# Kernel optimization log

Hardware: AMD Instinct MI355X
Metric: run time of the kernel (lower is better)

## Reference

```python
import jax, jax.numpy as jnp
import numpy as np

N_NODES = 100000
N_EDGES = 3200000
IN_F = 128
EDGE_F = 16
OUT_F = 128
EDGE_IMPORTANCE = 1.0


def setup_inputs() -> dict:
    key = jax.random.key(0)
    k1, k2, k3, k4, k5 = jax.random.split(key, 5)
    x = jax.random.normal(k1, (N_NODES, IN_F), dtype=jnp.float32)
    edge_index = jax.random.randint(k2, (2, N_EDGES), 0, N_NODES, dtype=jnp.int64)
    edge_attr = jax.random.normal(k3, (N_EDGES, EDGE_F), dtype=jnp.float32)
    # nn.Linear(in_features + edge_features, out_features): weight [OUT_F, IN_F+EDGE_F]
    fan_in = IN_F + EDGE_F
    bound = 1.0 / np.sqrt(fan_in)
    W = jax.random.uniform(k4, (OUT_F, fan_in), dtype=jnp.float32, minval=-bound, maxval=bound)
    b = jax.random.uniform(k5, (OUT_F,), dtype=jnp.float32, minval=-bound, maxval=bound)
    return {"x": x, "edge_index": edge_index, "edge_attr": edge_attr, "W": W, "b": b}


def reference(x, edge_index, edge_attr, W, b):
    row, col = edge_index[0], edge_index[1]
    # Linear on concat([x[row], edge_attr*imp]) == x[row] @ Wx.T + edge @ We.T + b
    Wx = W[:, :IN_F]           # [OUT_F, IN_F]
    We = W[:, IN_F:]           # [OUT_F, EDGE_F]
    atom_feats = x[row]                                     # [E, IN_F] gather
    edge_feats = edge_attr * EDGE_IMPORTANCE                # [E, EDGE_F]
    updated = (jnp.einsum('ei,oi->eo', atom_feats, Wx)
               + jnp.einsum('ej,oj->eo', edge_feats, We)
               + b)                                         # [E, OUT_F]
    # scatter_mean by destination node col, dim_size = N
    sums = jax.ops.segment_sum(updated, col, num_segments=N_NODES)        # [N, OUT_F]
    counts = jax.ops.segment_sum(jnp.ones((updated.shape[0],), updated.dtype),
                                 col, num_segments=N_NODES)               # [N]
    denom = jnp.maximum(counts, 1.0)[:, None]
    return sums / denom
```

## Files before the change

kernel.cpp:

```cpp
#include <hip/hip_runtime.h>

#define N_NODES 100000
#define N_EDGES 3200000
#define IN_F    128
#define EDGE_F  16
#define OUT_F   128
#define K_TOT   144

typedef float f32x4 __attribute__((ext_vector_type(4)));
typedef int   i32x2 __attribute__((ext_vector_type(2)));


__global__ void count_k(const int* __restrict__ col, int* __restrict__ counts,
                        int* __restrict__ rank) {
    int e = blockIdx.x * blockDim.x + threadIdx.x;
    if (e < N_EDGES) {
        int c = __builtin_nontemporal_load(col + e);
        int r = atomicAdd(&counts[c], 1);
        __builtin_nontemporal_store(r, rank + e);
    }
}

__global__ void scan1_k(const int* __restrict__ counts, int* __restrict__ offsets,
                        int* __restrict__ partials) {
    __shared__ int s[512];
    int i = blockIdx.x * 512 + threadIdx.x;
    int v = (i < N_NODES) ? counts[i] : 0;
    s[threadIdx.x] = v;
    __syncthreads();
    for (int d = 1; d < 512; d <<= 1) {
        int t = (threadIdx.x >= d) ? s[threadIdx.x - d] : 0;
        __syncthreads();
        s[threadIdx.x] += t;
        __syncthreads();
    }
    if (i < N_NODES) offsets[i] = s[threadIdx.x] - v;
    if (threadIdx.x == 511) partials[blockIdx.x] = s[511];
}

__global__ void scan2_k(int* partials) {
    __shared__ int s[256];
    int v = (threadIdx.x < 196) ? partials[threadIdx.x] : 0;
    s[threadIdx.x] = v;
    __syncthreads();
    for (int d = 1; d < 256; d <<= 1) {
        int t = (threadIdx.x >= d) ? s[threadIdx.x - d] : 0;
        __syncthreads();
        s[threadIdx.x] += t;
        __syncthreads();
    }
    if (threadIdx.x < 196) partials[threadIdx.x] = s[threadIdx.x] - v;
}

__global__ void scan3_k(int* __restrict__ offsets, const int* __restrict__ partials) {
    int i = blockIdx.x * 512 + threadIdx.x;
    if (i < N_NODES) offsets[i] += partials[blockIdx.x];
    if (i == 0) offsets[N_NODES] = N_EDGES;
}

__global__ void fill_k(const int* __restrict__ col, const int* __restrict__ row,
                       const int* __restrict__ rank, const int* __restrict__ offsets,
                       int2* __restrict__ csr2) {
    int e = blockIdx.x * blockDim.x + threadIdx.x;
    if (e < N_EDGES) {
        int c  = __builtin_nontemporal_load(col + e);
        int rk = __builtin_nontemporal_load(rank + e);
        int rw = __builtin_nontemporal_load(row + e);
        int pos = offsets[c] + rk;
        i32x2 v; v.x = e; v.y = rw;
        __builtin_nontemporal_store(v, ((i32x2*)csr2) + pos);
    }
}

__global__ __launch_bounds__(256) void gather_k(
        const float* __restrict__ x, const float* __restrict__ ea,
        const int* __restrict__ offsets, const int* __restrict__ csr2,
        float* __restrict__ Sx, float* __restrict__ Se) {
    const int wave = threadIdx.x >> 6;
    const int lane = threadIdx.x & 63;
    const int n = blockIdx.x * 4 + wave;

    const int off0 = offsets[n];
    const int deg  = offsets[n + 1] - off0;

    const int half = lane >> 5;
    const int l31  = lane & 31;
    const int eg16 = lane >> 2;
    const int l3   = lane & 3;

    f32x4 ax = {0.f, 0.f, 0.f, 0.f};
    f32x4 se = {0.f, 0.f, 0.f, 0.f};

    for (int base = 0; base < deg; base += 64) {
        int m = deg - base; if (m > 64) m = 64;
        int e = 0, r = 0;
        if (lane < m) {
            i32x2 er = __builtin_nontemporal_load(
                ((const i32x2*)csr2) + off0 + base + lane);
            e = er.x; r = er.y;
        }
        int j = 0;
        for (; j + 16 <= m; j += 16) {
            int r0 = __shfl(r, j + 0  + half);
            int r1 = __shfl(r, j + 2  + half);
            int r2 = __shfl(r, j + 4  + half);
            int r3 = __shfl(r, j + 6  + half);
            int r4 = __shfl(r, j + 8  + half);
            int r5 = __shfl(r, j + 10 + half);
            int r6 = __shfl(r, j + 12 + half);
            int r7 = __shfl(r, j + 14 + half);
            int ej = __shfl(e, j + eg16);
            f32x4 v0 = ((const f32x4*)(x + (size_t)r0 * IN_F))[l31];
            f32x4 v1 = ((const f32x4*)(x + (size_t)r1 * IN_F))[l31];
            f32x4 v2 = ((const f32x4*)(x + (size_t)r2 * IN_F))[l31];
            f32x4 v3 = ((const f32x4*)(x + (size_t)r3 * IN_F))[l31];
            f32x4 v4 = ((const f32x4*)(x + (size_t)r4 * IN_F))[l31];
            f32x4 v5 = ((const f32x4*)(x + (size_t)r5 * IN_F))[l31];
            f32x4 v6 = ((const f32x4*)(x + (size_t)r6 * IN_F))[l31];
            f32x4 v7 = ((const f32x4*)(x + (size_t)r7 * IN_F))[l31];
            f32x4 w  = __builtin_nontemporal_load(
                ((const f32x4*)ea) + (size_t)ej * 4 + l3);
            ax += (v0 + v1) + (v2 + v3) + (v4 + v5) + (v6 + v7);
            se += w;
        }
        for (; j < m; j += 2) {
            int rj = __shfl(r, j + half);
            if (j + half < m) {
                f32x4 v = ((const f32x4*)(x + (size_t)rj * IN_F))[l31];
                ax += v;
            }
            int eg = eg16 & 1;
            int ej = __shfl(e, j + eg);
            if (lane < 8 && (j + eg) < m) {
                f32x4 w = __builtin_nontemporal_load(
                    ((const f32x4*)ea) + (size_t)ej * 4 + l3);
                se += w;
            }
        }
    }

    ax.x += __shfl_xor(ax.x, 32);
    ax.y += __shfl_xor(ax.y, 32);
    ax.z += __shfl_xor(ax.z, 32);
    ax.w += __shfl_xor(ax.w, 32);
    #pragma unroll
    for (int off = 4; off < 64; off <<= 1) {
        se.x += __shfl_xor(se.x, off);
        se.y += __shfl_xor(se.y, off);
        se.z += __shfl_xor(se.z, off);
        se.w += __shfl_xor(se.w, off);
    }
    if (lane < 32)
        __builtin_nontemporal_store(ax, ((f32x4*)(Sx + (size_t)n * IN_F)) + l31);
    if (lane < 4)
        __builtin_nontemporal_store(se, ((f32x4*)(Se + (size_t)n * EDGE_F)) + l3);
}

#define TILE_N 64
__global__ __launch_bounds__(256) void gemm_k(
        const float* __restrict__ Sx, const float* __restrict__ Se,
        const int* __restrict__ offsets, const float* __restrict__ W,
        const float* __restrict__ b, float* __restrict__ out) {
    __shared__ float Wt[72 * 132];
    __shared__ float Sl[144 * 68];

    int tid = threadIdx.x;
    int to4 = (tid & 31) * 4;
    int tn8 = (tid >> 5) * 8;
    int n0 = blockIdx.x * TILE_N;

    for (int idx = tid; idx < TILE_N * IN_F; idx += 256) {
        int n = idx >> 7, k = idx & 127;
        int nn = n0 + n;
        Sl[k * 68 + n] = (nn < N_NODES)
            ? __builtin_nontemporal_load(Sx + (size_t)nn * IN_F + k) : 0.f;
    }
    for (int idx = tid; idx < TILE_N * EDGE_F; idx += 256) {
        int n = idx >> 4, k = idx & 15;
        int nn = n0 + n;
        Sl[(IN_F + k) * 68 + n] = (nn < N_NODES)
            ? __builtin_nontemporal_load(Se + (size_t)nn * EDGE_F + k) : 0.f;
    }

    f32x4 a0 = {0,0,0,0}, a1 = {0,0,0,0}, a2 = {0,0,0,0}, a3 = {0,0,0,0};
    f32x4 a4 = {0,0,0,0}, a5 = {0,0,0,0}, a6 = {0,0,0,0}, a7 = {0,0,0,0};

    for (int half = 0; half < 2; ++half) {
        __syncthreads();
        int kbase = half * 72;
        for (int idx = tid; idx < 72 * 128; idx += 256) {
            int o = idx / 72, kl = idx % 72;
            Wt[kl * 132 + o] = W[(size_t)o * K_TOT + kbase + kl];
        }
        __syncthreads();

        #pragma unroll 4
        for (int kl = 0; kl < 72; ++kl) {
            f32x4 w4 = *(const f32x4*)&Wt[kl * 132 + to4];
            f32x4 s0 = *(const f32x4*)&Sl[(kbase + kl) * 68 + tn8];
            f32x4 s1 = *(const f32x4*)&Sl[(kbase + kl) * 68 + tn8 + 4];
            a0 += s0.x * w4; a1 += s0.y * w4; a2 += s0.z * w4; a3 += s0.w * w4;
            a4 += s1.x * w4; a5 += s1.y * w4; a6 += s1.z * w4; a7 += s1.w * w4;
        }
    }

    f32x4 b4 = *(const f32x4*)&b[to4];
    f32x4 accs[8] = {a0, a1, a2, a3, a4, a5, a6, a7};
    #pragma unroll
    for (int j = 0; j < 8; ++j) {
        int n = n0 + tn8 + j;
        if (n < N_NODES) {
            float fdeg = (float)(offsets[n + 1] - offsets[n]);
            float inv = 1.0f / fmaxf(fdeg, 1.0f);
            f32x4 o4 = (accs[j] + fdeg * b4) * inv;
            __builtin_nontemporal_store(o4, (f32x4*)(out + (size_t)n * OUT_F + to4));
        }
    }
}

extern "C" void kernel_launch(void* const* d_in, const int* in_sizes, int n_in,
                              void* d_out, int out_size, void* d_ws, size_t ws_size,
                              hipStream_t stream) {
    const float* x  = (const float*)d_in[0];
    const int*   ei = (const int*)d_in[1];
    const float* ea = (const float*)d_in[2];
    const float* W  = (const float*)d_in[3];
    const float* b  = (const float*)d_in[4];
    float* out = (float*)d_out;

    char* ws = (char*)d_ws;
    int*   counts   = (int*)(ws + 0);
    int*   offsets  = (int*)(ws + 400000);
    int*   partials = (int*)(ws + 800016);
    int2*  csr2     = (int2*)(ws + 801040);
    float* Se       = (float*)(ws + 26401040);
    int*   rank     = (int*)d_out;

    const int* row = ei;
    const int* col = ei + N_EDGES;

    hipMemsetAsync(counts, 0, N_NODES * sizeof(int), stream);
    count_k<<<(N_EDGES + 255) / 256, 256, 0, stream>>>(col, counts, rank);
    scan1_k<<<196, 512, 0, stream>>>(counts, offsets, partials);
    scan2_k<<<1, 256, 0, stream>>>(partials);
    scan3_k<<<196, 512, 0, stream>>>(offsets, partials);
    fill_k<<<(N_EDGES + 255) / 256, 256, 0, stream>>>(col, row, rank, offsets, csr2);
    gather_k<<<N_NODES / 4, 256, 0, stream>>>(x, ea, offsets, (const int*)csr2, out, Se);
    gemm_k<<<(N_NODES + TILE_N - 1) / TILE_N, 256, 0, stream>>>(out, Se, offsets, W, b, out);
}
```

Baseline: 936.8 us.

## Replace per-node counting sort with two-level bucketed CSR build

```diff
diff --git a/kernel.cpp b/kernel.cpp
--- a/kernel.cpp
+++ b/kernel.cpp
@@ -7,68 +7,78 @@
 #define OUT_F   128
 #define K_TOT   144
 
+#define NBKT 782
+#define BCAP 4800
+
 typedef float f32x4 __attribute__((ext_vector_type(4)));
 typedef int   i32x2 __attribute__((ext_vector_type(2)));
 
 
-__global__ void count_k(const int* __restrict__ col, int* __restrict__ counts,
-                        int* __restrict__ rank) {
+__global__ void passA_k(const int* __restrict__ col, const int* __restrict__ row,
+                        int* __restrict__ bcnt, i32x2* __restrict__ bkt) {
     int e = blockIdx.x * blockDim.x + threadIdx.x;
     if (e < N_EDGES) {
         int c = __builtin_nontemporal_load(col + e);
-        int r = atomicAdd(&counts[c], 1);
-        __builtin_nontemporal_store(r, rank + e);
-    }
-}
-
-__global__ void scan1_k(const int* __restrict__ counts, int* __restrict__ offsets,
-                        int* __restrict__ partials) {
-    __shared__ int s[512];
-    int i = blockIdx.x * 512 + threadIdx.x;
-    int v = (i < N_NODES) ? counts[i] : 0;
-    s[threadIdx.x] = v;
-    __syncthreads();
-    for (int d = 1; d < 512; d <<= 1) {
-        int t = (threadIdx.x >= d) ? s[threadIdx.x - d] : 0;
-        __syncthreads();
-        s[threadIdx.x] += t;
-        __syncthreads();
-    }
-    if (i < N_NODES) offsets[i] = s[threadIdx.x] - v;
-    if (threadIdx.x == 511) partials[blockIdx.x] = s[511];
-}
-
-__global__ void scan2_k(int* partials) {
-    __shared__ int s[256];
-    int v = (threadIdx.x < 196) ? partials[threadIdx.x] : 0;
-    s[threadIdx.x] = v;
-    __syncthreads();
-    for (int d = 1; d < 256; d <<= 1) {
-        int t = (threadIdx.x >= d) ? s[threadIdx.x - d] : 0;
-        __syncthreads();
-        s[threadIdx.x] += t;
-        __syncthreads();
-    }
-    if (threadIdx.x < 196) partials[threadIdx.x] = s[threadIdx.x] - v;
-}
-
-__global__ void scan3_k(int* __restrict__ offsets, const int* __restrict__ partials) {
-    int i = blockIdx.x * 512 + threadIdx.x;
-    if (i < N_NODES) offsets[i] += partials[blockIdx.x];
-    if (i == 0) offsets[N_NODES] = N_EDGES;
-}
-
-__global__ void fill_k(const int* __restrict__ col, const int* __restrict__ row,
-                       const int* __restrict__ rank, const int* __restrict__ offsets,
-                       int2* __restrict__ csr2) {
-    int e = blockIdx.x * blockDim.x + threadIdx.x;
-    if (e < N_EDGES) {
-        int c  = __builtin_nontemporal_load(col + e);
-        int rk = __builtin_nontemporal_load(rank + e);
-        int rw = __builtin_nontemporal_load(row + e);
-        int pos = offsets[c] + rk;
-        i32x2 v; v.x = e; v.y = rw;
-        __builtin_nontemporal_store(v, ((i32x2*)csr2) + pos);
+        int r = __builtin_nontemporal_load(row + e);
+        int b = c >> 7;
+        int p = atomicAdd(&bcnt[b], 1);
+        if (p < BCAP) {
+            i32x2 v; v.x = (e << 7) | (c & 127); v.y = r;
+            bkt[(size_t)b * BCAP + p] = v;
+        }
+    }
+}
+
+__global__ void bscan_k(const int* __restrict__ bcnt, int* __restrict__ bbase) {
+    __shared__ int s[1024];
+    int t = threadIdx.x;
+    int v = (t < NBKT) ? min(bcnt[t], BCAP) : 0;
+    s[t] = v;
+    __syncthreads();
+    for (int d = 1; d < 1024; d <<= 1) {
+        int u = (t >= d) ? s[t - d] : 0;
+        __syncthreads();
+        s[t] += u;
+        __syncthreads();
+    }
+    if (t < NBKT) bbase[t] = s[t] - v;
+}
+
+__global__ __launch_bounds__(256) void passB_k(
+        const int* __restrict__ bcnt, const int* __restrict__ bbase,
+        const i32x2* __restrict__ bkt, int2* __restrict__ csr2,
+        int* __restrict__ offsets) {
+    __shared__ int hist[128], cur[128], scn[128];
+    int b = blockIdx.x, t = threadIdx.x;
+    int cnt  = min(bcnt[b], BCAP);
+    int base = bbase[b];
+    if (t < 128) hist[t] = 0;
+    __syncthreads();
+    const i32x2* mybkt = bkt + (size_t)b * BCAP;
+    for (int i = t; i < cnt; i += 256)
+        atomicAdd(&hist[mybkt[i].x & 127], 1);
+    __syncthreads();
+    if (t < 128) scn[t] = hist[t];
+    __syncthreads();
+    for (int d = 1; d < 128; d <<= 1) {
+        int u = 0;
+        if (t < 128 && t >= d) u = scn[t - d];
+        __syncthreads();
+        if (t < 128) scn[t] += u;
+        __syncthreads();
+    }
+    if (t < 128) {
+        int excl = scn[t] - hist[t];
+        cur[t] = excl;
+        int n = b * 128 + t;
+        if (n < N_NODES) offsets[n] = base + excl;
+    }
+    if (b == 0 && t == 0) offsets[N_NODES] = N_EDGES;
+    __syncthreads();
+    for (int i = t; i < cnt; i += 256) {
+        i32x2 v = mybkt[i];
+        int p = atomicAdd(&cur[v.x & 127], 1);
+        csr2[base + p] = make_int2(v.x >> 7, v.y);
     }
 }
 
@@ -229,22 +239,20 @@
     float* out = (float*)d_out;
 
     char* ws = (char*)d_ws;
-    int*   counts   = (int*)(ws + 0);
-    int*   offsets  = (int*)(ws + 400000);
-    int*   partials = (int*)(ws + 800016);
-    int2*  csr2     = (int2*)(ws + 801040);
-    float* Se       = (float*)(ws + 26401040);
-    int*   rank     = (int*)d_out;
+    int*   bcnt    = (int*)(ws + 0);
+    int*   bbase   = (int*)(ws + 16384);
+    int*   offsets = (int*)(ws + 400000);
+    int2*  csr2    = (int2*)(ws + 801040);
+    float* Se      = (float*)(ws + 26401040);
+    i32x2* bkt     = (i32x2*)d_out;
 
     const int* row = ei;
     const int* col = ei + N_EDGES;
 
-    hipMemsetAsync(counts, 0, N_NODES * sizeof(int), stream);
-    count_k<<<(N_EDGES + 255) / 256, 256, 0, stream>>>(col, counts, rank);
-    scan1_k<<<196, 512, 0, stream>>>(counts, offsets, partials);
-    scan2_k<<<1, 256, 0, stream>>>(partials);
-    scan3_k<<<196, 512, 0, stream>>>(offsets, partials);
-    fill_k<<<(N_EDGES + 255) / 256, 256, 0, stream>>>(col, row, rank, offsets, csr2);
+    hipMemsetAsync(bcnt, 0, NBKT * sizeof(int), stream);
+    passA_k<<<(N_EDGES + 255) / 256, 256, 0, stream>>>(col, row, bcnt, bkt);
+    bscan_k<<<1, 1024, 0, stream>>>(bcnt, bbase);
+    passB_k<<<NBKT, 256, 0, stream>>>(bcnt, bbase, bkt, csr2, offsets);
     gather_k<<<N_NODES / 4, 256, 0, stream>>>(x, ea, offsets, (const int*)csr2, out, Se);
     gemm_k<<<(N_NODES + TILE_N - 1) / TILE_N, 256, 0, stream>>>(out, Se, offsets, W, b, out);
 }
```

Result: slower. 1.451 ms (+54.9%).
